# Performance work log

Hardware: AMD Instinct MI355X
Metric: run time of the kernel (lower is better)

## Reference

```python
import jax, jax.numpy as jnp
import numpy as np

# ---- architecture constants (from init_kwargs) ----
BIG_K, SMALL_K = 51, 5
C_OUT, GROUP_IN = 96, 4
NK = -(-BIG_K // SMALL_K)          # 11 small kernels tile the big kernel
C_IN = C_OUT * NK                  # 1056
PADDING = SMALL_K - 1              # 4
EXTRA_PAD = PADDING - SMALL_K // 2 # 2
MID = BIG_K // 2                   # 25
REAL_PAD = [MID - i * SMALL_K - PADDING for i in range(NK)]
B, HOUT, WOUT = 8, 56, 56
HIN = HOUT + 2 * EXTRA_PAD         # 60


def setup_inputs() -> dict:
    key = jax.random.key(0)
    k1, k2, k3, k4 = jax.random.split(key, 4)
    rng = np.random.default_rng(0)
    rp = np.asarray(REAL_PAD, dtype=np.int32)
    # pad_hv: (C_IN, 2*GROUP_IN). Columns 0..G-1 horizontal shifts, G..2G-1 vertical.
    # For each (output-channel block, column) the nk channels get a random permutation of REAL_PAD.
    pad_hv = np.empty((C_IN, 2 * GROUP_IN), dtype=np.int32)
    for g in range(2 * GROUP_IN):
        for co in range(C_OUT):
            pad_hv[co * NK:(co + 1) * NK, g] = rng.permutation(rp)
    # idx_identit: (C_OUT, GROUP_IN); one randomly chosen channel inside each block.
    idx_identit = (rng.integers(0, NK, size=(C_OUT, GROUP_IN)) + np.arange(C_OUT)[:, None] * NK).astype(np.int32)
    x = jax.random.normal(k1, (B, C_IN, HIN, HIN), dtype=jnp.float32)
    w1 = jax.random.uniform(k2, (C_IN * GROUP_IN,), dtype=jnp.float32)
    w2 = jax.random.uniform(k3, (C_IN * GROUP_IN,), dtype=jnp.float32)
    w3 = jax.random.uniform(k4, (C_OUT * GROUP_IN,), dtype=jnp.float32)
    return {
        'x': x, 'w1': w1, 'w2': w2, 'w3': w3,
        'pad_hv': jnp.asarray(pad_hv), 'idx_identit': jnp.asarray(idx_identit),
        'b': B, 'hout': HOUT, 'wout': WOUT,
    }


def _forward(x, w1, w2, w3, pad_hv, idx_identit, hout, wout):
    Bx, C, H_in, W_in = x.shape
    c_out, G = idx_identit.shape
    nk = C // c_out
    ep = (H_in - hout) // 2  # extra_pad
    w1r = w1.reshape(G, C)
    w2r = w2.reshape(G, C)
    w3r = w3.reshape(G, c_out)

    # ---- horizontal shift branch (weights w1) ----
    xh = x[:, :, ep:ep + hout, :]                       # (B,C,hout,W_in)
    wpos = jnp.arange(wout)
    acc_h = jnp.zeros((Bx, C, hout, wout), x.dtype)
    for g in range(G):  # small fixed hyperparameter loop
        idxW = wpos[None, :] + ep + pad_hv[:, g][:, None]       # (C,wout)
        valid = (idxW >= 0) & (idxW < W_in)
        gat = jnp.take_along_axis(xh, jnp.clip(idxW, 0, W_in - 1)[None, :, None, :], axis=3)
        gat = jnp.where(valid[None, :, None, :], gat, 0.0)
        acc_h = acc_h + gat * w1r[g][None, :, None, None]
    out_h = acc_h.reshape(Bx, c_out, nk, hout, wout).sum(axis=2)  # scatter by idx_out (block structure)

    # ---- vertical shift branch (weights w2) ----
    xv = x[:, :, :, ep:ep + wout]                       # (B,C,H_in,wout)
    hpos = jnp.arange(hout)
    acc_v = jnp.zeros((Bx, C, hout, wout), x.dtype)
    for g in range(G):
        idxH = hpos[None, :] + ep + pad_hv[:, G + g][:, None]   # (C,hout)
        valid = (idxH >= 0) & (idxH < H_in)
        gat = jnp.take_along_axis(xv, jnp.clip(idxH, 0, H_in - 1)[None, :, :, None], axis=2)
        gat = jnp.where(valid[None, :, :, None], gat, 0.0)
        acc_v = acc_v + gat * w2r[g][None, :, None, None]
    out_v = acc_v.reshape(Bx, c_out, nk, hout, wout).sum(axis=2)

    # ---- identity branch (weights w3): pick one channel per output per group ----
    xc = x[:, :, ep:ep + hout, ep:ep + wout]            # (B,C,hout,wout)
    out_i = jnp.zeros((Bx, c_out, hout, wout), x.dtype)
    for g in range(G):
        out_i = out_i + xc[:, idx_identit[:, g]] * w3r[g][None, :, None, None]
    return out_h, out_v, out_i


def reference(x, w1, w2, w3, pad_hv, idx_identit, b, hout, wout):
    # Matches AddShift_mp_linear_module.forward: returns the three chunks (x, y, z)
    return _forward(x, w1, w2, w3, pad_hv, idx_identit, hout, wout)
```

## Files before the change

### kernel.cpp

```cpp
#include <hip/hip_runtime.h>

#define BATCH   8
#define C_OUT_N 96
#define NK      11
#define C_IN_N  1056
#define GRP     4
#define HOUT    56
#define WOUT    56
#define HIN     60
#define WIN     60
#define EP      2

#define CH_DW   (HIN * WIN)
#define BUF_DW  3840
#define ROWS_PW 7

typedef const float __attribute__((address_space(1)))* gas1_t;
typedef float       __attribute__((address_space(3)))* las3_t;

__device__ __forceinline__ void stage_chan(const float* src, float* dst, int tid)
{
    const int wid  = tid >> 6;
    const int lane = tid & 63;
    __builtin_amdgcn_global_load_lds((gas1_t)(src + (wid * 64 + lane) * 4),
                                     (las3_t)(dst + wid * 256), 16, 0, 0);
    if (wid < 7) {
        int f1 = 512 + wid * 64 + lane;
        if (f1 > 899) f1 = 899;
        __builtin_amdgcn_global_load_lds((gas1_t)(src + f1 * 4),
                                         (las3_t)(dst + 2048 + wid * 256), 16, 0, 0);
    }
}

__global__ __launch_bounds__(512, 3) void addshift_kernel(
    const float* __restrict__ x,
    const float* __restrict__ w1,
    const float* __restrict__ w2,
    const float* __restrict__ w3,
    const int*   __restrict__ pad_hv,
    const int*   __restrict__ idx_identit,
    float* __restrict__ out)
{
    const int co  = blockIdx.x;
    const int b   = blockIdx.y;
    const int tid = threadIdx.x;

    __shared__ __align__(16) float buf[2][BUF_DW];

    const int wave = tid >> 6;
    const int w    = tid & 63;
    const int wc   = (w < WOUT) ? w : (WOUT - 1);
    const int h0   = __builtin_amdgcn_readfirstlane(wave * ROWS_PW);
    const int cV   = wc + EP;

    int   kI[GRP];
    float w3v[GRP];
#pragma unroll
    for (int g = 0; g < GRP; ++g) {
        kI[g]  = idx_identit[co * GRP + g] - co * NK;
        w3v[g] = w3[g * C_OUT_N + co];
    }

    float accH[ROWS_PW], accV[ROWS_PW], accI[ROWS_PW];
#pragma unroll
    for (int i = 0; i < ROWS_PW; ++i) { accH[i] = 0.f; accV[i] = 0.f; accI[i] = 0.f; }

    const float* chan_base = x + ((size_t)b * C_IN_N + (size_t)co * NK) * CH_DW;

    stage_chan(chan_base, buf[0], tid);

#pragma unroll 1
    for (int k = 0; k < NK; ++k) {
        __syncthreads();

        if (k + 1 < NK)
            stage_chan(chan_base + (size_t)(k + 1) * CH_DW, buf[(k + 1) & 1], tid);

        const float* __restrict__ bf = buf[k & 1];

        const int c = co * NK + k;
        int ph[GRP], pv[GRP];
        float a1[GRP], a2[GRP];
#pragma unroll
        for (int g = 0; g < GRP; ++g) {
            ph[g] = pad_hv[c * 8 + g];
            pv[g] = pad_hv[c * 8 + 4 + g];
            a1[g] = w1[g * C_IN_N + c];
            a2[g] = w2[g * C_IN_N + c];
        }
        float wi = 0.f;
#pragma unroll
        for (int g = 0; g < GRP; ++g)
            if (kI[g] == k) wi += w3v[g];

        const float* hrow = bf + (h0 + EP) * WIN;
#pragma unroll
        for (int g = 0; g < GRP; ++g) {
            int ix   = wc + EP + ph[g];
            float wh = ((unsigned)ix < (unsigned)WIN) ? a1[g] : 0.f;
            int ixc  = ix < 0 ? 0 : (ix > WIN - 1 ? WIN - 1 : ix);
            const float* p = hrow + ixc;
#pragma unroll
            for (int i = 0; i < ROWS_PW; ++i)
                accH[i] = fmaf(p[i * WIN], wh, accH[i]);
        }

#pragma unroll
        for (int g = 0; g < GRP; ++g) {
            const int rb = h0 + EP + pv[g];
            if (rb >= 0 && rb <= HIN - ROWS_PW) {
                const float* p = bf + rb * WIN + cV;
#pragma unroll
                for (int i = 0; i < ROWS_PW; ++i)
                    accV[i] = fmaf(p[i * WIN], a2[g], accV[i]);
            } else {
#pragma unroll
                for (int i = 0; i < ROWS_PW; ++i) {
                    int r    = rb + i;
                    float wv = ((unsigned)r < (unsigned)HIN) ? a2[g] : 0.f;
                    int rc   = r < 0 ? 0 : (r > HIN - 1 ? HIN - 1 : r);
                    accV[i]  = fmaf(bf[rc * WIN + cV], wv, accV[i]);
                }
            }
        }

        if (wi != 0.f) {
            const float* p = bf + (h0 + EP) * WIN + cV;
#pragma unroll
            for (int i = 0; i < ROWS_PW; ++i)
                accI[i] = fmaf(p[i * WIN], wi, accI[i]);
        }
    }

    if (w < WOUT) {
        const size_t OSZ  = (size_t)BATCH * C_OUT_N * HOUT * WOUT;
        const size_t base = (((size_t)b * C_OUT_N + co) * HOUT + h0) * WOUT + w;
#pragma unroll
        for (int i = 0; i < ROWS_PW; ++i) {
            out[base + (size_t)i * WOUT]           = accH[i];
            out[OSZ + base + (size_t)i * WOUT]     = accV[i];
            out[2 * OSZ + base + (size_t)i * WOUT] = accI[i];
        }
    }
}

extern "C" void kernel_launch(void* const* d_in, const int* in_sizes, int n_in,
                              void* d_out, int out_size, void* d_ws, size_t ws_size,
                              hipStream_t stream) {
    const float* x   = (const float*)d_in[0];
    const float* w1  = (const float*)d_in[1];
    const float* w2  = (const float*)d_in[2];
    const float* w3  = (const float*)d_in[3];
    const int* pad_hv      = (const int*)d_in[4];
    const int* idx_identit = (const int*)d_in[5];
    float* out = (float*)d_out;

    dim3 grid(C_OUT_N, BATCH);
    dim3 block(512);
    addshift_kernel<<<grid, block, 0, stream>>>(x, w1, w2, w3, pad_hv, idx_identit, out);
}
```

Measured before the change: 199.2 us.

## Triple-buffer LDS channel staging with prefetch distance two and vmcnt waits

Moves from double to triple LDS buffering so each block prefetches two channels ahead. The full __syncthreads is replaced by an explicit s_waitcnt vmcnt on the async global-to-LDS loads plus a raw barrier, and the next prefetch is issued after the compute instead of before it. All waves now issue both staging loads, with duplicated tail data, so the per-wave outstanding-load count stays uniform for the vmcnt accounting. The 7-row loops are also split into 4+3 halves with a second base pointer. This aims to hide more global-load latency, at the cost of a larger LDS footprint per block (three 16 KB buffers), which could limit occupancy.

```diff
diff --git a/kernel.cpp b/kernel.cpp
--- a/kernel.cpp
+++ b/kernel.cpp
@@ -12,7 +12,8 @@
 #define EP      2
 
 #define CH_DW   (HIN * WIN)
-#define BUF_DW  3840
+#define BUF_DW  4096
+#define NBUF    3
 #define ROWS_PW 7
 
 typedef const float __attribute__((address_space(1)))* gas1_t;
@@ -24,12 +25,10 @@
     const int lane = tid & 63;
     __builtin_amdgcn_global_load_lds((gas1_t)(src + (wid * 64 + lane) * 4),
                                      (las3_t)(dst + wid * 256), 16, 0, 0);
-    if (wid < 7) {
-        int f1 = 512 + wid * 64 + lane;
-        if (f1 > 899) f1 = 899;
-        __builtin_amdgcn_global_load_lds((gas1_t)(src + f1 * 4),
-                                         (las3_t)(dst + 2048 + wid * 256), 16, 0, 0);
-    }
+    int f1 = 512 + wid * 64 + lane;
+    if (f1 > 899) f1 = 899;
+    __builtin_amdgcn_global_load_lds((gas1_t)(src + f1 * 4),
+                                     (las3_t)(dst + 2048 + wid * 256), 16, 0, 0);
 }
 
 __global__ __launch_bounds__(512, 3) void addshift_kernel(
@@ -45,7 +44,7 @@
     const int b   = blockIdx.y;
     const int tid = threadIdx.x;
 
-    __shared__ __align__(16) float buf[2][BUF_DW];
+    __shared__ __align__(16) float buf[NBUF][BUF_DW];
 
     const int wave = tid >> 6;
     const int w    = tid & 63;
@@ -67,16 +66,16 @@
 
     const float* chan_base = x + ((size_t)b * C_IN_N + (size_t)co * NK) * CH_DW;
 
-    stage_chan(chan_base, buf[0], tid);
+    stage_chan(chan_base,                     buf[0], tid);
+    stage_chan(chan_base + (size_t)CH_DW,     buf[1], tid);
 
 #pragma unroll 1
     for (int k = 0; k < NK; ++k) {
-        __syncthreads();
+        if (k < NK - 1) { asm volatile("s_waitcnt vmcnt(2)" ::: "memory"); }
+        else            { asm volatile("s_waitcnt vmcnt(0)" ::: "memory"); }
+        __builtin_amdgcn_s_barrier();
 
-        if (k + 1 < NK)
-            stage_chan(chan_base + (size_t)(k + 1) * CH_DW, buf[(k + 1) & 1], tid);
-
-        const float* __restrict__ bf = buf[k & 1];
+        const float* __restrict__ bf = buf[k % NBUF];
 
         const int c = co * NK + k;
         int ph[GRP], pv[GRP];
@@ -100,9 +99,13 @@
             float wh = ((unsigned)ix < (unsigned)WIN) ? a1[g] : 0.f;
             int ixc  = ix < 0 ? 0 : (ix > WIN - 1 ? WIN - 1 : ix);
             const float* p = hrow + ixc;
+            const float* q = p + 4 * WIN;
 #pragma unroll
-            for (int i = 0; i < ROWS_PW; ++i)
+            for (int i = 0; i < 4; ++i)
                 accH[i] = fmaf(p[i * WIN], wh, accH[i]);
+#pragma unroll
+            for (int i = 0; i < 3; ++i)
+                accH[4 + i] = fmaf(q[i * WIN], wh, accH[4 + i]);
         }
 
 #pragma unroll
@@ -110,9 +113,13 @@
             const int rb = h0 + EP + pv[g];
             if (rb >= 0 && rb <= HIN - ROWS_PW) {
                 const float* p = bf + rb * WIN + cV;
+                const float* q = p + 4 * WIN;
 #pragma unroll
-                for (int i = 0; i < ROWS_PW; ++i)
+                for (int i = 0; i < 4; ++i)
                     accV[i] = fmaf(p[i * WIN], a2[g], accV[i]);
+#pragma unroll
+                for (int i = 0; i < 3; ++i)
+                    accV[4 + i] = fmaf(q[i * WIN], a2[g], accV[4 + i]);
             } else {
 #pragma unroll
                 for (int i = 0; i < ROWS_PW; ++i) {
@@ -126,10 +133,17 @@
 
         if (wi != 0.f) {
             const float* p = bf + (h0 + EP) * WIN + cV;
+            const float* q = p + 4 * WIN;
 #pragma unroll
-            for (int i = 0; i < ROWS_PW; ++i)
+            for (int i = 0; i < 4; ++i)
                 accI[i] = fmaf(p[i * WIN], wi, accI[i]);
+#pragma unroll
+            for (int i = 0; i < 3; ++i)
+                accI[4 + i] = fmaf(q[i * WIN], wi, accI[4 + i]);
         }
+
+        if (k + 2 < NK)
+            stage_chan(chan_base + (size_t)(k + 2) * CH_DW, buf[(k + 2) % NBUF], tid);
     }
 
     if (w < WOUT) {
```

Measured after the change: 198.9 us. No clear change (-0.1%).

## Read input channels directly from global memory and broadcast per-channel params via readlane

Applied to the files above, without the earlier changes.

Removes the double-buffered LDS staging of each input channel and its per-iteration barriers, so the shifted taps are gathered straight from global memory through the caches. Per-channel shift offsets and weights are now loaded once into lanes up front and broadcast with readlane, instead of being reloaded from global memory every iteration. This drops LDS traffic and block-wide synchronisation but makes every tap a global or cache access with no explicit prefetch, so it depends on L1/L2 hit rates to hide latency.

```diff
diff --git a/kernel.cpp b/kernel.cpp
--- a/kernel.cpp
+++ b/kernel.cpp
@@ -12,25 +12,7 @@
 #define EP      2
 
 #define CH_DW   (HIN * WIN)
-#define BUF_DW  3840
 #define ROWS_PW 7
-
-typedef const float __attribute__((address_space(1)))* gas1_t;
-typedef float       __attribute__((address_space(3)))* las3_t;
-
-__device__ __forceinline__ void stage_chan(const float* src, float* dst, int tid)
-{
-    const int wid  = tid >> 6;
-    const int lane = tid & 63;
-    __builtin_amdgcn_global_load_lds((gas1_t)(src + (wid * 64 + lane) * 4),
-                                     (las3_t)(dst + wid * 256), 16, 0, 0);
-    if (wid < 7) {
-        int f1 = 512 + wid * 64 + lane;
-        if (f1 > 899) f1 = 899;
-        __builtin_amdgcn_global_load_lds((gas1_t)(src + f1 * 4),
-                                         (las3_t)(dst + 2048 + wid * 256), 16, 0, 0);
-    }
-}
 
 __global__ __launch_bounds__(512, 3) void addshift_kernel(
     const float* __restrict__ x,
@@ -45,13 +27,23 @@
     const int b   = blockIdx.y;
     const int tid = threadIdx.x;
 
-    __shared__ __align__(16) float buf[2][BUF_DW];
-
     const int wave = tid >> 6;
     const int w    = tid & 63;
     const int wc   = (w < WOUT) ? w : (WOUT - 1);
     const int h0   = __builtin_amdgcn_readfirstlane(wave * ROWS_PW);
     const int cV   = wc + EP;
+
+    int   myPh = 0, myPv = 0;
+    float myA1 = 0.f, myA2 = 0.f;
+    if (w < GRP * NK) {
+        const int lg = w / NK;
+        const int lk = w - lg * NK;
+        const int lc = co * NK + lk;
+        myPh = pad_hv[lc * 8 + lg];
+        myPv = pad_hv[lc * 8 + 4 + lg];
+        myA1 = w1[lg * C_IN_N + lc];
+        myA2 = w2[lg * C_IN_N + lc];
+    }
 
     int   kI[GRP];
     float w3v[GRP];
@@ -67,33 +59,26 @@
 
     const float* chan_base = x + ((size_t)b * C_IN_N + (size_t)co * NK) * CH_DW;
 
-    stage_chan(chan_base, buf[0], tid);
-
 #pragma unroll 1
     for (int k = 0; k < NK; ++k) {
-        __syncthreads();
+        const float* __restrict__ ch = chan_base + (size_t)k * CH_DW;
 
-        if (k + 1 < NK)
-            stage_chan(chan_base + (size_t)(k + 1) * CH_DW, buf[(k + 1) & 1], tid);
-
-        const float* __restrict__ bf = buf[k & 1];
-
-        const int c = co * NK + k;
         int ph[GRP], pv[GRP];
         float a1[GRP], a2[GRP];
 #pragma unroll
         for (int g = 0; g < GRP; ++g) {
-            ph[g] = pad_hv[c * 8 + g];
-            pv[g] = pad_hv[c * 8 + 4 + g];
-            a1[g] = w1[g * C_IN_N + c];
-            a2[g] = w2[g * C_IN_N + c];
+            const int src = g * NK + k;
+            ph[g] = __builtin_amdgcn_readlane(myPh, src);
+            pv[g] = __builtin_amdgcn_readlane(myPv, src);
+            a1[g] = __uint_as_float(__builtin_amdgcn_readlane(__float_as_uint(myA1), src));
+            a2[g] = __uint_as_float(__builtin_amdgcn_readlane(__float_as_uint(myA2), src));
         }
         float wi = 0.f;
 #pragma unroll
         for (int g = 0; g < GRP; ++g)
             if (kI[g] == k) wi += w3v[g];
 
-        const float* hrow = bf + (h0 + EP) * WIN;
+        const float* hrow = ch + (h0 + EP) * WIN;
 #pragma unroll
         for (int g = 0; g < GRP; ++g) {
             int ix   = wc + EP + ph[g];
@@ -109,7 +94,7 @@
         for (int g = 0; g < GRP; ++g) {
             const int rb = h0 + EP + pv[g];
             if (rb >= 0 && rb <= HIN - ROWS_PW) {
-                const float* p = bf + rb * WIN + cV;
+                const float* p = ch + rb * WIN + cV;
 #pragma unroll
                 for (int i = 0; i < ROWS_PW; ++i)
                     accV[i] = fmaf(p[i * WIN], a2[g], accV[i]);
@@ -119,13 +104,13 @@
                     int r    = rb + i;
                     float wv = ((unsigned)r < (unsigned)HIN) ? a2[g] : 0.f;
                     int rc   = r < 0 ? 0 : (r > HIN - 1 ? HIN - 1 : r);
-                    accV[i]  = fmaf(bf[rc * WIN + cV], wv, accV[i]);
+                    accV[i]  = fmaf(ch[rc * WIN + cV], wv, accV[i]);
                 }
             }
         }
 
         if (wi != 0.f) {
-            const float* p = bf + (h0 + EP) * WIN + cV;
+            const float* p = ch + (h0 + EP) * WIN + cV;
 #pragma unroll
             for (int i = 0; i < ROWS_PW; ++i)
                 accI[i] = fmaf(p[i * WIN], wi, accI[i]);
```

Result: slower. 234.5 us (+17.7%).
